# Kernel optimization log

Hardware: AMD Instinct MI355X
Metric: run time of the kernel (lower is better)

## Reference

```python
import jax, jax.numpy as jnp
import numpy as np

N, E = 100_000, 1_600_000
C_IN = C_OUT = 2


def _ln(h, g, b, eps=1e-5):
    mu = h.mean(-1, keepdims=True)
    var = ((h - mu) ** 2).mean(-1, keepdims=True)
    return (h - mu) * jax.lax.rsqrt(var + eps) * g + b


def _radial(x, W1, b1, g1, be1, W2, b2, g2, be2, W3, b3):
    h = jax.nn.relu(_ln(x @ W1 + b1, g1, be1))
    h = jax.nn.relu(_ln(h @ W2 + b2, g2, be2))
    return h @ W3 + b3


def setup_inputs() -> dict:
    key = jax.random.key(0)
    ks = jax.random.split(key, 20)
    inp = {
        "f0": jax.random.normal(ks[0], (N, C_IN, 1), jnp.float32),
        "f1": jax.random.normal(ks[1], (N, C_IN, 3), jnp.float32),
        "dist": jax.random.uniform(ks[2], (E,), jnp.float32),
        "u": jax.random.randint(ks[3], (E,), 0, N),
        "v": jax.random.randint(ks[4], (E,), 0, N),
        "wq": 0.5 * jax.random.normal(ks[5], (2, C_OUT, C_IN), jnp.float32),
        "wj00": jax.random.normal(ks[6], (E, 1, 1, 1), jnp.float32),
        "wj01": jax.random.normal(ks[7], (E, 1, 1, 3), jnp.float32),
        "wj10": jax.random.normal(ks[8], (E, 1, 3, 1), jnp.float32),
        "wj11": jax.random.normal(ks[9], (E, 3, 3, 3), jnp.float32),
        # radial MLP params for the 4 WLayers, index i = 2*l + k
        "rW1": 0.5 * jax.random.normal(ks[10], (4, C_IN + 1, 16), jnp.float32),
        "rb1": jnp.zeros((4, 16), jnp.float32),
        "g1": jnp.ones((4, 16), jnp.float32),
        "be1": jnp.zeros((4, 16), jnp.float32),
        "rW2": 0.3 * jax.random.normal(ks[11], (4, 16, 16), jnp.float32),
        "rb2": jnp.zeros((4, 16), jnp.float32),
        "g2": jnp.ones((4, 16), jnp.float32),
        "be2": jnp.zeros((4, 16), jnp.float32),
        "W3_00": 0.3 * jax.random.normal(ks[12], (16, 4), jnp.float32),
        "b3_00": jnp.zeros((4,), jnp.float32),
        "W3_01": 0.3 * jax.random.normal(ks[13], (16, 4), jnp.float32),
        "b3_01": jnp.zeros((4,), jnp.float32),
        "W3_10": 0.3 * jax.random.normal(ks[14], (16, 4), jnp.float32),
        "b3_10": jnp.zeros((4,), jnp.float32),
        "W3_11": 0.3 * jax.random.normal(ks[15], (16, 12), jnp.float32),
        "b3_11": jnp.zeros((12,), jnp.float32),
    }
    return inp


def reference(f0, f1, dist, u, v, wq, wj00, wj01, wj10, wj11,
              rW1, rb1, g1, be1, rW2, rb2, g2, be2,
              W3_00, b3_00, W3_01, b3_01, W3_10, b3_10, W3_11, b3_11):
    n = f0.shape[0]
    e = u.shape[0]
    # calc_q: [N, c_out, sum(2k+1)=4]
    q = jnp.concatenate([jnp.einsum('oi,nik->nok', wq[0], f0),
                         jnp.einsum('oi,nik->nok', wq[1], f1)], axis=2)
    # per-edge radial input: [dot(f0_src, f0_dst) over rep dim, dist] -> [E, c_in+1]
    vec = jnp.concatenate([jnp.sum(f0[u] * f0[v], axis=2), dist[:, None]], axis=1)
    f_dst = (f0[v], f1[v])  # edges.dst[k]
    wjs = {(0, 0): wj00, (0, 1): wj01, (1, 0): wj10, (1, 1): wj11}
    W3s = {(0, 0): (W3_00, b3_00), (0, 1): (W3_01, b3_01),
           (1, 0): (W3_10, b3_10), (1, 1): (W3_11, b3_11)}
    # calc_k: for each output degree l, sum over input degrees k of
    #   einsum('ejoi,ejlk,eik->eol', R, w_j, f_dst[k])  (fused form of the
    #   original 'ejoi,ejlk->eoilk' then 'eoilk,eik->eol')
    kl = []
    for l in range(2):
        acc = jnp.zeros((e, C_OUT, 2 * l + 1), f0.dtype)
        for k in range(2):
            i = 2 * l + k
            W3, b3 = W3s[(l, k)]
            J = 2 * min(k, l) + 1
            R = _radial(vec, rW1[i], rb1[i], g1[i], be1[i],
                        rW2[i], rb2[i], g2[i], be2[i], W3, b3)
            R = R.reshape(e, J, C_OUT, C_IN)
            acc = acc + jnp.einsum('ejoi,ejlk,eik->eol', R, wjs[(l, k)], f_dst[k])
        kl.append(acc)
    k_feat = jnp.concatenate(kl, axis=2)  # [E, c_out, 4]
    dot = jnp.einsum('eol,eol->e', q[v], k_feat)  # [E]
    # scatter logsumexp over destination nodes, then edge softmax weights
    m = jax.lax.stop_gradient(jax.ops.segment_max(dot, v, num_segments=n))
    m = jnp.where(jnp.isfinite(m), m, 0.0)
    ssum = jax.ops.segment_sum(jnp.exp(dot - m[v]), v, num_segments=n)
    lse = m + jnp.log(ssum)
    return jnp.exp(dot - lse[v])
```

## Files before the change

### kernel.cpp

```cpp
#include <hip/hip_runtime.h>
#include <math.h>


#define TPB 256
#define EPB 128

typedef float f2 __attribute__((ext_vector_type(2)));
typedef float f4 __attribute__((ext_vector_type(4)));

static __device__ __forceinline__ f2 fma2(f2 a, f2 b, f2 c) {
    return __builtin_elementwise_fma(a, b, c);
}
static __device__ __forceinline__ f2 splat(float x) {
    f2 r;
    r.x = x;
    r.y = x;
    return r;
}
static __device__ __forceinline__ f2 mk2(float a, float b) {
    f2 r;
    r.x = a;
    r.y = b;
    return r;
}

static __device__ __forceinline__ void ln_relu_pair(f2* h,
                                                    const float* __restrict__ g,
                                                    const float* __restrict__ be) {
    f2 s = ((h[0] + h[1]) + (h[2] + h[3])) + ((h[4] + h[5]) + (h[6] + h[7])) +
           (((h[8] + h[9]) + (h[10] + h[11])) +
            ((h[12] + h[13]) + (h[14] + h[15])));
    const f2 mu = s * splat(0.0625f);
    f2 vs = splat(0.f);
#pragma unroll
    for (int c = 0; c < 16; ++c) {
        f2 d = h[c] - mu;
        vs = fma2(d, d, vs);
    }
    const f2 var = vs * splat(0.0625f);
    f2 r;
    r.x = rsqrtf(var.x + 1e-5f);
    r.y = rsqrtf(var.y + 1e-5f);
    const f2 zero = splat(0.f);
#pragma unroll
    for (int c = 0; c < 16; ++c) {
        f2 t = (h[c] - mu) * r;
        h[c] = __builtin_elementwise_max(fma2(t, splat(g[c]), splat(be[c])), zero);
    }
}

static __device__ __forceinline__ void radial_pair(
    f2 v0, f2 v1, f2 v2, const float* __restrict__ W1,
    const float* __restrict__ b1, const float* __restrict__ g1,
    const float* __restrict__ be1, const float* __restrict__ W2,
    const float* __restrict__ b2, const float* __restrict__ g2,
    const float* __restrict__ be2, f2* h2) {
    f2 h[16];
#pragma unroll
    for (int c = 0; c < 16; ++c)
        h[c] = fma2(v0, splat(W1[c]),
                    fma2(v1, splat(W1[16 + c]),
                         fma2(v2, splat(W1[32 + c]), splat(b1[c]))));
    ln_relu_pair(h, g1, be1);

#pragma unroll
    for (int c2 = 0; c2 < 16; ++c2) h2[c2] = splat(b2[c2]);
#pragma unroll
    for (int c = 0; c < 16; ++c) {
#pragma unroll
        for (int c2 = 0; c2 < 16; ++c2)
            h2[c2] = fma2(h[c], splat(W2[c * 16 + c2]), h2[c2]);
    }
    ln_relu_pair(h2, g2, be2);
}

static __device__ __forceinline__ void layer3_pair4(const f2* h2,
                                                    const float* __restrict__ W3,
                                                    const float* __restrict__ b3,
                                                    f2 p[4]) {
#pragma unroll
    for (int oi = 0; oi < 4; ++oi) p[oi] = splat(b3[oi]);
#pragma unroll
    for (int c = 0; c < 16; ++c) {
#pragma unroll
        for (int oi = 0; oi < 4; ++oi)
            p[oi] = fma2(h2[c], splat(W3[c * 4 + oi]), p[oi]);
    }
}

__global__ __launch_bounds__(TPB, 4) void edge_kernel(
    const float* __restrict__ f0, const float* __restrict__ f1,
    const float* __restrict__ dist, const int* __restrict__ u,
    const int* __restrict__ v, const float* __restrict__ wq,
    const float* __restrict__ wj00, const float* __restrict__ wj01,
    const float* __restrict__ wj10, const float* __restrict__ wj11,
    const float* __restrict__ rW1, const float* __restrict__ rb1,
    const float* __restrict__ g1, const float* __restrict__ be1,
    const float* __restrict__ rW2, const float* __restrict__ rb2,
    const float* __restrict__ g2, const float* __restrict__ be2,
    const float* __restrict__ W3_00, const float* __restrict__ b3_00,
    const float* __restrict__ W3_01, const float* __restrict__ b3_01,
    const float* __restrict__ W3_10, const float* __restrict__ b3_10,
    const float* __restrict__ W3_11, const float* __restrict__ b3_11,
    float* __restrict__ out, double* __restrict__ ssum, int E) {
    __shared__ __align__(16) float s11[EPB * 27];
    __shared__ __align__(16) float s01[EPB * 3];
    __shared__ __align__(16) float s10[EPB * 3];
    __shared__ __align__(16) float sprep[EPB * 12];
    __shared__ int sv[EPB];
    __shared__ f2 pdot[4][64];

    const int tid = threadIdx.x;
    const int base = blockIdx.x * EPB;
    const int rem = E - base;
    const int nE = (rem < EPB) ? rem : EPB;

    if (nE == EPB) {
        const f4* s11s = (const f4*)(wj11 + (size_t)base * 27);
        f4* s11d = (f4*)s11;
#pragma unroll 2
        for (int i = tid; i < EPB * 27 / 4; i += TPB) s11d[i] = s11s[i];
        if (tid < EPB * 3 / 4) {
            ((f4*)s01)[tid] = ((const f4*)(wj01 + (size_t)base * 3))[tid];
            ((f4*)s10)[tid] = ((const f4*)(wj10 + (size_t)base * 3))[tid];
        }
    } else {
        for (int i = tid; i < EPB * 27; i += TPB)
            s11[i] = (i < nE * 27) ? wj11[(size_t)base * 27 + i] : 0.f;
        for (int i = tid; i < EPB * 3; i += TPB) {
            s01[i] = (i < nE * 3) ? wj01[(size_t)base * 3 + i] : 0.f;
            s10[i] = (i < nE * 3) ? wj10[(size_t)base * 3 + i] : 0.f;
        }
    }

    if (tid < EPB) {
        const int e = base + tid;
        f4 t0 = {0.f, 0.f, 0.f, 0.f};
        f4 t1 = {0.f, 0.f, 0.f, 0.f};
        f4 t2 = {0.f, 0.f, 0.f, 0.f};
        int vv = 0;
        if (e < E) {
            const int uu = u[e];
            vv = v[e];
            const f2 f0u = *(const f2*)(f0 + (size_t)uu * 2);
            const f2 f0v2 = *(const f2*)(f0 + (size_t)vv * 2);
            const f2 f1a = *(const f2*)(f1 + (size_t)vv * 6);
            const f2 f1b = *(const f2*)(f1 + (size_t)vv * 6 + 2);
            const f2 f1c = *(const f2*)(f1 + (size_t)vv * 6 + 4);
            const float d = dist[e];
            t0.x = f0u.x * f0v2.x;
            t0.y = f0u.y * f0v2.y;
            t0.z = d;
            t0.w = f0v2.x;
            t1.x = f0v2.y;
            t1.y = f1a.x;
            t1.z = f1a.y;
            t1.w = f1b.x;
            t2.x = f1b.y;
            t2.y = f1c.x;
            t2.z = f1c.y;
        }
        f4* dst = (f4*)(sprep + tid * 12);
        dst[0] = t0;
        dst[1] = t1;
        dst[2] = t2;
        sv[tid] = vv;
    }
    __syncthreads();

    const int l = tid & 63;
    const int w = __builtin_amdgcn_readfirstlane(tid >> 6);

    const float* pA = sprep + l * 12;
    const float* pB = sprep + (l + 64) * 12;
#define PR(k) mk2(pA[k], pB[k])
    const f2 vec0 = PR(0);
    const f2 vec1 = PR(1);
    const f2 vec2 = PR(2);
    const f2 f0v0 = PR(3);
    const f2 f0v1 = PR(4);
    f2 f1v[2][3];
    if (w != 0) {
        f1v[0][0] = PR(5);
        f1v[0][1] = PR(6);
        f1v[0][2] = PR(7);
        f1v[1][0] = PR(8);
        f1v[1][1] = PR(9);
        f1v[1][2] = PR(10);
    }
#undef PR

    f2 h2[16];
    radial_pair(vec0, vec1, vec2, rW1 + w * 48, rb1 + w * 16, g1 + w * 16,
                be1 + w * 16, rW2 + w * 256, rb2 + w * 16, g2 + w * 16,
                be2 + w * 16, h2);

    f2 dotp = splat(0.f);
    if (w == 0) {
        f2 p[4];
        layer3_pair4(h2, W3_00, b3_00, p);
        const int eA = base + l, eB = eA + 64;
        f2 wj;
        wj.x = (eA < E) ? wj00[eA] : 0.f;
        wj.y = (eB < E) ? wj00[eB] : 0.f;
        const f2 a0 = wj * fma2(p[0], f0v0, p[1] * f0v1);
        const f2 a1 = wj * fma2(p[2], f0v0, p[3] * f0v1);
        const f2 q00 = fma2(splat(wq[0]), f0v0, splat(wq[1]) * f0v1);
        const f2 q01 = fma2(splat(wq[2]), f0v0, splat(wq[3]) * f0v1);
        dotp = fma2(q00, a0, q01 * a1);
    } else if (w == 1) {
        f2 p[4];
        layer3_pair4(h2, W3_01, b3_01, p);
        const float* mA = s01 + l * 3;
        const float* mB = s01 + (l + 64) * 3;
        f2 s0 = splat(0.f), s1 = splat(0.f);
#pragma unroll
        for (int m = 0; m < 3; ++m) {
            const f2 wm = mk2(mA[m], mB[m]);
            s0 = fma2(wm, f1v[0][m], s0);
            s1 = fma2(wm, f1v[1][m], s1);
        }
        const f2 a0 = fma2(p[0], s0, p[1] * s1);
        const f2 a1 = fma2(p[2], s0, p[3] * s1);
        const f2 q00 = fma2(splat(wq[0]), f0v0, splat(wq[1]) * f0v1);
        const f2 q01 = fma2(splat(wq[2]), f0v0, splat(wq[3]) * f0v1);
        dotp = fma2(q00, a0, q01 * a1);
    } else if (w == 2) {
        f2 p[4];
        layer3_pair4(h2, W3_10, b3_10, p);
        const f2 t0 = fma2(p[0], f0v0, p[1] * f0v1);
        const f2 t1 = fma2(p[2], f0v0, p[3] * f0v1);
        const float* mA = s10 + l * 3;
        const float* mB = s10 + (l + 64) * 3;
#pragma unroll
        for (int m = 0; m < 3; ++m) {
            const f2 wm = mk2(mA[m], mB[m]);
            const f2 q0 = fma2(splat(wq[4]), f1v[0][m], splat(wq[5]) * f1v[1][m]);
            const f2 q1 = fma2(splat(wq[6]), f1v[0][m], splat(wq[7]) * f1v[1][m]);
            dotp = fma2(q0 * wm, t0, dotp);
            dotp = fma2(q1 * wm, t1, dotp);
        }
    } else {
        f2 p[3][4];
#pragma unroll
        for (int j = 0; j < 3; ++j)
#pragma unroll
            for (int oi = 0; oi < 4; ++oi) p[j][oi] = splat(b3_11[j * 4 + oi]);
#pragma unroll
        for (int c = 0; c < 16; ++c) {
#pragma unroll
            for (int j = 0; j < 3; ++j)
#pragma unroll
                for (int oi = 0; oi < 4; ++oi)
                    p[j][oi] = fma2(h2[c], splat(W3_11[c * 12 + j * 4 + oi]),
                                    p[j][oi]);
        }
        const float* mA = s11 + l * 27;
        const float* mB = s11 + (l + 64) * 27;
        f2 acc1[2][3];
#pragma unroll
        for (int m = 0; m < 3; ++m) {
            acc1[0][m] = splat(0.f);
            acc1[1][m] = splat(0.f);
        }
#pragma unroll
        for (int j = 0; j < 3; ++j) {
#pragma unroll
            for (int m = 0; m < 3; ++m) {
                const f2 w0 = mk2(mA[j * 9 + m * 3 + 0], mB[j * 9 + m * 3 + 0]);
                const f2 w1 = mk2(mA[j * 9 + m * 3 + 1], mB[j * 9 + m * 3 + 1]);
                const f2 w2 = mk2(mA[j * 9 + m * 3 + 2], mB[j * 9 + m * 3 + 2]);
                const f2 B0 =
                    fma2(w0, f1v[0][0], fma2(w1, f1v[0][1], w2 * f1v[0][2]));
                const f2 B1 =
                    fma2(w0, f1v[1][0], fma2(w1, f1v[1][1], w2 * f1v[1][2]));
                acc1[0][m] = fma2(p[j][0], B0, fma2(p[j][1], B1, acc1[0][m]));
                acc1[1][m] = fma2(p[j][2], B0, fma2(p[j][3], B1, acc1[1][m]));
            }
        }
#pragma unroll
        for (int m = 0; m < 3; ++m) {
            const f2 q0 = fma2(splat(wq[4]), f1v[0][m], splat(wq[5]) * f1v[1][m]);
            const f2 q1 = fma2(splat(wq[6]), f1v[0][m], splat(wq[7]) * f1v[1][m]);
            dotp = fma2(q0, acc1[0][m], dotp);
            dotp = fma2(q1, acc1[1][m], dotp);
        }
    }

    pdot[w][l] = dotp;
    __syncthreads();

    if (w == 0) {
        const f2 d =
            (pdot[0][l] + pdot[1][l]) + (pdot[2][l] + pdot[3][l]);
        const int eA = base + l, eB = eA + 64;
        if (eA < E) {
            out[eA] = d.x;
            atomicAdd(&ssum[sv[l]], exp((double)d.x));
        }
        if (eB < E) {
            out[eB] = d.y;
            atomicAdd(&ssum[sv[l + 64]], exp((double)d.y));
        }
    }
}

__global__ void norm_kernel(float* __restrict__ out, const int* __restrict__ v,
                            const double* __restrict__ ssum, int E) {
    int e = blockIdx.x * blockDim.x + threadIdx.x;
    if (e >= E) return;
    const double t = exp((double)out[e]);
    out[e] = (float)(t / ssum[v[e]]);
}

extern "C" void kernel_launch(void* const* d_in, const int* in_sizes, int n_in,
                              void* d_out, int out_size, void* d_ws,
                              size_t ws_size, hipStream_t stream) {
    const float* f0 = (const float*)d_in[0];
    const float* f1 = (const float*)d_in[1];
    const float* dist = (const float*)d_in[2];
    const int* u = (const int*)d_in[3];
    const int* v = (const int*)d_in[4];
    const float* wq = (const float*)d_in[5];
    const float* wj00 = (const float*)d_in[6];
    const float* wj01 = (const float*)d_in[7];
    const float* wj10 = (const float*)d_in[8];
    const float* wj11 = (const float*)d_in[9];
    const float* rW1 = (const float*)d_in[10];
    const float* rb1 = (const float*)d_in[11];
    const float* g1 = (const float*)d_in[12];
    const float* be1 = (const float*)d_in[13];
    const float* rW2 = (const float*)d_in[14];
    const float* rb2 = (const float*)d_in[15];
    const float* g2 = (const float*)d_in[16];
    const float* be2 = (const float*)d_in[17];
    const float* W3_00 = (const float*)d_in[18];
    const float* b3_00 = (const float*)d_in[19];
    const float* W3_01 = (const float*)d_in[20];
    const float* b3_01 = (const float*)d_in[21];
    const float* W3_10 = (const float*)d_in[22];
    const float* b3_10 = (const float*)d_in[23];
    const float* W3_11 = (const float*)d_in[24];
    const float* b3_11 = (const float*)d_in[25];

    const int N = in_sizes[0] / 2;
    const int E = in_sizes[2];

    double* ssum = (double*)d_ws;
    float* out = (float*)d_out;

    hipMemsetAsync(ssum, 0, (size_t)N * sizeof(double), stream);
    const int ge = (E + EPB - 1) / EPB;
    edge_kernel<<<ge, TPB, 0, stream>>>(
        f0, f1, dist, u, v, wq, wj00, wj01, wj10, wj11, rW1, rb1, g1, be1, rW2,
        rb2, g2, be2, W3_00, b3_00, W3_01, b3_01, W3_10, b3_10, W3_11, b3_11,
        out, ssum, E);
    const int gn = (E + TPB - 1) / TPB;
    norm_kernel<<<gn, TPB, 0, stream>>>(out, v, ssum, E);
}
```

Measured before the change: 406.1 us.

## Halve block to two waves, each computing two radial MLPs interleaved

The edge block drops from four wavefronts (one radial MLP each) to two. Each wave evaluates two radial MLPs side by side: wave 0 pairs (0,0) with (1,1), wave 1 pairs (0,1) with (1,0), which balances the heavier 11 path. The interleaved dual MLP is meant to give more independent FMAs per thread for ILP. The prep shared buffer becomes structure-of-arrays so all 128 threads write it without bank conflicts. The trade is higher register pressure and a lower occupancy hint (3 instead of 4), with less wave-level parallelism per edge tile.

```diff
diff --git a/kernel.cpp b/kernel.cpp
--- a/kernel.cpp
+++ b/kernel.cpp
@@ -2,7 +2,7 @@
 #include <math.h>
 
 
-#define TPB 256
+#define TPB 128
 #define EPB 128
 
 typedef float f2 __attribute__((ext_vector_type(2)));
@@ -24,54 +24,77 @@
     return r;
 }
 
-static __device__ __forceinline__ void ln_relu_pair(f2* h,
-                                                    const float* __restrict__ g,
-                                                    const float* __restrict__ be) {
-    f2 s = ((h[0] + h[1]) + (h[2] + h[3])) + ((h[4] + h[5]) + (h[6] + h[7])) +
-           (((h[8] + h[9]) + (h[10] + h[11])) +
-            ((h[12] + h[13]) + (h[14] + h[15])));
-    const f2 mu = s * splat(0.0625f);
-    f2 vs = splat(0.f);
-#pragma unroll
-    for (int c = 0; c < 16; ++c) {
-        f2 d = h[c] - mu;
-        vs = fma2(d, d, vs);
-    }
-    const f2 var = vs * splat(0.0625f);
-    f2 r;
-    r.x = rsqrtf(var.x + 1e-5f);
-    r.y = rsqrtf(var.y + 1e-5f);
+static __device__ __forceinline__ void ln_relu_dual(
+    f2* a, const float* __restrict__ ga, const float* __restrict__ ba,
+    f2* b, const float* __restrict__ gb, const float* __restrict__ bb) {
+    f2 sa = ((a[0] + a[1]) + (a[2] + a[3])) + ((a[4] + a[5]) + (a[6] + a[7])) +
+            (((a[8] + a[9]) + (a[10] + a[11])) +
+             ((a[12] + a[13]) + (a[14] + a[15])));
+    f2 sb = ((b[0] + b[1]) + (b[2] + b[3])) + ((b[4] + b[5]) + (b[6] + b[7])) +
+            (((b[8] + b[9]) + (b[10] + b[11])) +
+             ((b[12] + b[13]) + (b[14] + b[15])));
+    const f2 mua = sa * splat(0.0625f);
+    const f2 mub = sb * splat(0.0625f);
+    f2 va = splat(0.f), vb = splat(0.f);
+#pragma unroll
+    for (int c = 0; c < 16; ++c) {
+        f2 da = a[c] - mua;
+        f2 db = b[c] - mub;
+        va = fma2(da, da, va);
+        vb = fma2(db, db, vb);
+    }
+    const f2 vara = va * splat(0.0625f);
+    const f2 varb = vb * splat(0.0625f);
+    f2 ra, rb;
+    ra.x = rsqrtf(vara.x + 1e-5f);
+    ra.y = rsqrtf(vara.y + 1e-5f);
+    rb.x = rsqrtf(varb.x + 1e-5f);
+    rb.y = rsqrtf(varb.y + 1e-5f);
     const f2 zero = splat(0.f);
 #pragma unroll
     for (int c = 0; c < 16; ++c) {
-        f2 t = (h[c] - mu) * r;
-        h[c] = __builtin_elementwise_max(fma2(t, splat(g[c]), splat(be[c])), zero);
-    }
-}
-
-static __device__ __forceinline__ void radial_pair(
-    f2 v0, f2 v1, f2 v2, const float* __restrict__ W1,
-    const float* __restrict__ b1, const float* __restrict__ g1,
-    const float* __restrict__ be1, const float* __restrict__ W2,
-    const float* __restrict__ b2, const float* __restrict__ g2,
-    const float* __restrict__ be2, f2* h2) {
-    f2 h[16];
-#pragma unroll
-    for (int c = 0; c < 16; ++c)
-        h[c] = fma2(v0, splat(W1[c]),
-                    fma2(v1, splat(W1[16 + c]),
-                         fma2(v2, splat(W1[32 + c]), splat(b1[c]))));
-    ln_relu_pair(h, g1, be1);
-
-#pragma unroll
-    for (int c2 = 0; c2 < 16; ++c2) h2[c2] = splat(b2[c2]);
-#pragma unroll
-    for (int c = 0; c < 16; ++c) {
-#pragma unroll
-        for (int c2 = 0; c2 < 16; ++c2)
-            h2[c2] = fma2(h[c], splat(W2[c * 16 + c2]), h2[c2]);
-    }
-    ln_relu_pair(h2, g2, be2);
+        f2 ta = (a[c] - mua) * ra;
+        f2 tb = (b[c] - mub) * rb;
+        a[c] = __builtin_elementwise_max(fma2(ta, splat(ga[c]), splat(ba[c])), zero);
+        b[c] = __builtin_elementwise_max(fma2(tb, splat(gb[c]), splat(bb[c])), zero);
+    }
+}
+
+static __device__ __forceinline__ void radial_dual(
+    f2 v0, f2 v1, f2 v2, const float* __restrict__ W1A,
+    const float* __restrict__ b1A, const float* __restrict__ g1A,
+    const float* __restrict__ be1A, const float* __restrict__ W2A,
+    const float* __restrict__ b2A, const float* __restrict__ g2A,
+    const float* __restrict__ be2A, const float* __restrict__ W1B,
+    const float* __restrict__ b1B, const float* __restrict__ g1B,
+    const float* __restrict__ be1B, const float* __restrict__ W2B,
+    const float* __restrict__ b2B, const float* __restrict__ g2B,
+    const float* __restrict__ be2B, f2* h2a, f2* h2b) {
+    f2 ha[16], hb[16];
+#pragma unroll
+    for (int c = 0; c < 16; ++c) {
+        ha[c] = fma2(v0, splat(W1A[c]),
+                     fma2(v1, splat(W1A[16 + c]),
+                          fma2(v2, splat(W1A[32 + c]), splat(b1A[c]))));
+        hb[c] = fma2(v0, splat(W1B[c]),
+                     fma2(v1, splat(W1B[16 + c]),
+                          fma2(v2, splat(W1B[32 + c]), splat(b1B[c]))));
+    }
+    ln_relu_dual(ha, g1A, be1A, hb, g1B, be1B);
+#pragma unroll
+    for (int c2 = 0; c2 < 16; ++c2) {
+        h2a[c2] = splat(b2A[c2]);
+        h2b[c2] = splat(b2B[c2]);
+    }
+#pragma unroll
+    for (int c = 0; c < 16; ++c) {
+#pragma unroll
+        for (int c2 = 0; c2 < 16; ++c2) {
+            h2a[c2] = fma2(ha[c], splat(W2A[c * 16 + c2]), h2a[c2]);
+            h2b[c2] = fma2(hb[c], splat(W2B[c * 16 + c2]), h2b[c2]);
+        }
+    }
+    ln_relu_dual(h2a, g2A, be2A, h2b, g2B, be2B);
 }
 
 static __device__ __forceinline__ void layer3_pair4(const f2* h2,
@@ -88,7 +111,7 @@
     }
 }
 
-__global__ __launch_bounds__(TPB, 4) void edge_kernel(
+__global__ __launch_bounds__(TPB, 3) void edge_kernel(
     const float* __restrict__ f0, const float* __restrict__ f1,
     const float* __restrict__ dist, const int* __restrict__ u,
     const int* __restrict__ v, const float* __restrict__ wq,
@@ -106,9 +129,9 @@
     __shared__ __align__(16) float s11[EPB * 27];
     __shared__ __align__(16) float s01[EPB * 3];
     __shared__ __align__(16) float s10[EPB * 3];
-    __shared__ __align__(16) float sprep[EPB * 12];
+    __shared__ float sprep[11][EPB];
     __shared__ int sv[EPB];
-    __shared__ f2 pdot[4][64];
+    __shared__ f2 pdot[2][64];
 
     const int tid = threadIdx.x;
     const int base = blockIdx.x * EPB;
@@ -118,7 +141,6 @@
     if (nE == EPB) {
         const f4* s11s = (const f4*)(wj11 + (size_t)base * 27);
         f4* s11d = (f4*)s11;
-#pragma unroll 2
         for (int i = tid; i < EPB * 27 / 4; i += TPB) s11d[i] = s11s[i];
         if (tid < EPB * 3 / 4) {
             ((f4*)s01)[tid] = ((const f4*)(wj01 + (size_t)base * 3))[tid];
@@ -133,11 +155,11 @@
         }
     }
 
-    if (tid < EPB) {
+    {
         const int e = base + tid;
-        f4 t0 = {0.f, 0.f, 0.f, 0.f};
-        f4 t1 = {0.f, 0.f, 0.f, 0.f};
-        f4 t2 = {0.f, 0.f, 0.f, 0.f};
+        float p[11];
+#pragma unroll
+        for (int k = 0; k < 11; ++k) p[k] = 0.f;
         int vv = 0;
         if (e < E) {
             const int uu = u[e];
@@ -147,23 +169,20 @@
             const f2 f1a = *(const f2*)(f1 + (size_t)vv * 6);
             const f2 f1b = *(const f2*)(f1 + (size_t)vv * 6 + 2);
             const f2 f1c = *(const f2*)(f1 + (size_t)vv * 6 + 4);
-            const float d = dist[e];
-            t0.x = f0u.x * f0v2.x;
-            t0.y = f0u.y * f0v2.y;
-            t0.z = d;
-            t0.w = f0v2.x;
-            t1.x = f0v2.y;
-            t1.y = f1a.x;
-            t1.z = f1a.y;
-            t1.w = f1b.x;
-            t2.x = f1b.y;
-            t2.y = f1c.x;
-            t2.z = f1c.y;
-        }
-        f4* dst = (f4*)(sprep + tid * 12);
-        dst[0] = t0;
-        dst[1] = t1;
-        dst[2] = t2;
+            p[0] = f0u.x * f0v2.x;
+            p[1] = f0u.y * f0v2.y;
+            p[2] = dist[e];
+            p[3] = f0v2.x;
+            p[4] = f0v2.y;
+            p[5] = f1a.x;
+            p[6] = f1a.y;
+            p[7] = f1b.x;
+            p[8] = f1b.y;
+            p[9] = f1c.x;
+            p[10] = f1c.y;
+        }
+#pragma unroll
+        for (int k = 0; k < 11; ++k) sprep[k][tid] = p[k];
         sv[tid] = vv;
     }
     __syncthreads();
@@ -171,119 +190,132 @@
     const int l = tid & 63;
     const int w = __builtin_amdgcn_readfirstlane(tid >> 6);
 
-    const float* pA = sprep + l * 12;
-    const float* pB = sprep + (l + 64) * 12;
-#define PR(k) mk2(pA[k], pB[k])
-    const f2 vec0 = PR(0);
-    const f2 vec1 = PR(1);
-    const f2 vec2 = PR(2);
-    const f2 f0v0 = PR(3);
-    const f2 f0v1 = PR(4);
+    const int iA = w;
+    const int iB = 3 - w;
+
+    const f2 vec0 = mk2(sprep[0][l], sprep[0][l + 64]);
+    const f2 vec1 = mk2(sprep[1][l], sprep[1][l + 64]);
+    const f2 vec2 = mk2(sprep[2][l], sprep[2][l + 64]);
+
+    f2 h2a[16], h2b[16];
+    radial_dual(vec0, vec1, vec2,
+                rW1 + iA * 48, rb1 + iA * 16, g1 + iA * 16, be1 + iA * 16,
+                rW2 + iA * 256, rb2 + iA * 16, g2 + iA * 16, be2 + iA * 16,
+                rW1 + iB * 48, rb1 + iB * 16, g1 + iB * 16, be1 + iB * 16,
+                rW2 + iB * 256, rb2 + iB * 16, g2 + iB * 16, be2 + iB * 16,
+                h2a, h2b);
+
+    const f2 f0v0 = mk2(sprep[3][l], sprep[3][l + 64]);
+    const f2 f0v1 = mk2(sprep[4][l], sprep[4][l + 64]);
     f2 f1v[2][3];
-    if (w != 0) {
-        f1v[0][0] = PR(5);
-        f1v[0][1] = PR(6);
-        f1v[0][2] = PR(7);
-        f1v[1][0] = PR(8);
-        f1v[1][1] = PR(9);
-        f1v[1][2] = PR(10);
-    }
-#undef PR
-
-    f2 h2[16];
-    radial_pair(vec0, vec1, vec2, rW1 + w * 48, rb1 + w * 16, g1 + w * 16,
-                be1 + w * 16, rW2 + w * 256, rb2 + w * 16, g2 + w * 16,
-                be2 + w * 16, h2);
-
+    f1v[0][0] = mk2(sprep[5][l], sprep[5][l + 64]);
+    f1v[0][1] = mk2(sprep[6][l], sprep[6][l + 64]);
+    f1v[0][2] = mk2(sprep[7][l], sprep[7][l + 64]);
+    f1v[1][0] = mk2(sprep[8][l], sprep[8][l + 64]);
+    f1v[1][1] = mk2(sprep[9][l], sprep[9][l + 64]);
+    f1v[1][2] = mk2(sprep[10][l], sprep[10][l + 64]);
+
+    const int eA = base + l, eB = eA + 64;
     f2 dotp = splat(0.f);
+
     if (w == 0) {
-        f2 p[4];
-        layer3_pair4(h2, W3_00, b3_00, p);
-        const int eA = base + l, eB = eA + 64;
-        f2 wj;
-        wj.x = (eA < E) ? wj00[eA] : 0.f;
-        wj.y = (eB < E) ? wj00[eB] : 0.f;
-        const f2 a0 = wj * fma2(p[0], f0v0, p[1] * f0v1);
-        const f2 a1 = wj * fma2(p[2], f0v0, p[3] * f0v1);
-        const f2 q00 = fma2(splat(wq[0]), f0v0, splat(wq[1]) * f0v1);
-        const f2 q01 = fma2(splat(wq[2]), f0v0, splat(wq[3]) * f0v1);
-        dotp = fma2(q00, a0, q01 * a1);
-    } else if (w == 1) {
-        f2 p[4];
-        layer3_pair4(h2, W3_01, b3_01, p);
-        const float* mA = s01 + l * 3;
-        const float* mB = s01 + (l + 64) * 3;
-        f2 s0 = splat(0.f), s1 = splat(0.f);
-#pragma unroll
-        for (int m = 0; m < 3; ++m) {
-            const f2 wm = mk2(mA[m], mB[m]);
-            s0 = fma2(wm, f1v[0][m], s0);
-            s1 = fma2(wm, f1v[1][m], s1);
-        }
-        const f2 a0 = fma2(p[0], s0, p[1] * s1);
-        const f2 a1 = fma2(p[2], s0, p[3] * s1);
-        const f2 q00 = fma2(splat(wq[0]), f0v0, splat(wq[1]) * f0v1);
-        const f2 q01 = fma2(splat(wq[2]), f0v0, splat(wq[3]) * f0v1);
-        dotp = fma2(q00, a0, q01 * a1);
-    } else if (w == 2) {
-        f2 p[4];
-        layer3_pair4(h2, W3_10, b3_10, p);
-        const f2 t0 = fma2(p[0], f0v0, p[1] * f0v1);
-        const f2 t1 = fma2(p[2], f0v0, p[3] * f0v1);
-        const float* mA = s10 + l * 3;
-        const float* mB = s10 + (l + 64) * 3;
-#pragma unroll
-        for (int m = 0; m < 3; ++m) {
-            const f2 wm = mk2(mA[m], mB[m]);
-            const f2 q0 = fma2(splat(wq[4]), f1v[0][m], splat(wq[5]) * f1v[1][m]);
-            const f2 q1 = fma2(splat(wq[6]), f1v[0][m], splat(wq[7]) * f1v[1][m]);
-            dotp = fma2(q0 * wm, t0, dotp);
-            dotp = fma2(q1 * wm, t1, dotp);
+        {
+            f2 p[4];
+            layer3_pair4(h2a, W3_00, b3_00, p);
+            f2 wj;
+            wj.x = (eA < E) ? wj00[eA] : 0.f;
+            wj.y = (eB < E) ? wj00[eB] : 0.f;
+            const f2 a0 = wj * fma2(p[0], f0v0, p[1] * f0v1);
+            const f2 a1 = wj * fma2(p[2], f0v0, p[3] * f0v1);
+            const f2 q00 = fma2(splat(wq[0]), f0v0, splat(wq[1]) * f0v1);
+            const f2 q01 = fma2(splat(wq[2]), f0v0, splat(wq[3]) * f0v1);
+            dotp = fma2(q00, a0, q01 * a1);
+        }
+        {
+            f2 p[3][4];
+#pragma unroll
+            for (int j = 0; j < 3; ++j)
+#pragma unroll
+                for (int oi = 0; oi < 4; ++oi)
+                    p[j][oi] = splat(b3_11[j * 4 + oi]);
+#pragma unroll
+            for (int c = 0; c < 16; ++c) {
+#pragma unroll
+                for (int j = 0; j < 3; ++j)
+#pragma unroll
+                    for (int oi = 0; oi < 4; ++oi)
+                        p[j][oi] = fma2(h2b[c], splat(W3_11[c * 12 + j * 4 + oi]),
+                                        p[j][oi]);
+            }
+            const float* mA = s11 + l * 27;
+            const float* mB = s11 + (l + 64) * 27;
+            f2 acc1[2][3];
+#pragma unroll
+            for (int m = 0; m < 3; ++m) {
+                acc1[0][m] = splat(0.f);
+                acc1[1][m] = splat(0.f);
+            }
+#pragma unroll
+            for (int j = 0; j < 3; ++j) {
+#pragma unroll
+                for (int m = 0; m < 3; ++m) {
+                    const f2 w0 = mk2(mA[j * 9 + m * 3 + 0], mB[j * 9 + m * 3 + 0]);
+                    const f2 w1 = mk2(mA[j * 9 + m * 3 + 1], mB[j * 9 + m * 3 + 1]);
+                    const f2 w2 = mk2(mA[j * 9 + m * 3 + 2], mB[j * 9 + m * 3 + 2]);
+                    const f2 B0 =
+                        fma2(w0, f1v[0][0], fma2(w1, f1v[0][1], w2 * f1v[0][2]));
+                    const f2 B1 =
+                        fma2(w0, f1v[1][0], fma2(w1, f1v[1][1], w2 * f1v[1][2]));
+                    acc1[0][m] = fma2(p[j][0], B0, fma2(p[j][1], B1, acc1[0][m]));
+                    acc1[1][m] = fma2(p[j][2], B0, fma2(p[j][3], B1, acc1[1][m]));
+                }
+            }
+#pragma unroll
+            for (int m = 0; m < 3; ++m) {
+                const f2 q0 =
+                    fma2(splat(wq[4]), f1v[0][m], splat(wq[5]) * f1v[1][m]);
+                const f2 q1 =
+                    fma2(splat(wq[6]), f1v[0][m], splat(wq[7]) * f1v[1][m]);
+                dotp = fma2(q0, acc1[0][m], dotp);
+                dotp = fma2(q1, acc1[1][m], dotp);
+            }
         }
     } else {
-        f2 p[3][4];
-#pragma unroll
-        for (int j = 0; j < 3; ++j)
-#pragma unroll
-            for (int oi = 0; oi < 4; ++oi) p[j][oi] = splat(b3_11[j * 4 + oi]);
-#pragma unroll
-        for (int c = 0; c < 16; ++c) {
-#pragma unroll
-            for (int j = 0; j < 3; ++j)
-#pragma unroll
-                for (int oi = 0; oi < 4; ++oi)
-                    p[j][oi] = fma2(h2[c], splat(W3_11[c * 12 + j * 4 + oi]),
-                                    p[j][oi]);
-        }
-        const float* mA = s11 + l * 27;
-        const float* mB = s11 + (l + 64) * 27;
-        f2 acc1[2][3];
-#pragma unroll
-        for (int m = 0; m < 3; ++m) {
-            acc1[0][m] = splat(0.f);
-            acc1[1][m] = splat(0.f);
-        }
-#pragma unroll
-        for (int j = 0; j < 3; ++j) {
+        {
+            f2 p[4];
+            layer3_pair4(h2a, W3_01, b3_01, p);
+            const float* mA = s01 + l * 3;
+            const float* mB = s01 + (l + 64) * 3;
+            f2 s0 = splat(0.f), s1 = splat(0.f);
 #pragma unroll
             for (int m = 0; m < 3; ++m) {
-                const f2 w0 = mk2(mA[j * 9 + m * 3 + 0], mB[j * 9 + m * 3 + 0]);
-                const f2 w1 = mk2(mA[j * 9 + m * 3 + 1], mB[j * 9 + m * 3 + 1]);
-                const f2 w2 = mk2(mA[j * 9 + m * 3 + 2], mB[j * 9 + m * 3 + 2]);
-                const f2 B0 =
-                    fma2(w0, f1v[0][0], fma2(w1, f1v[0][1], w2 * f1v[0][2]));
-                const f2 B1 =
-                    fma2(w0, f1v[1][0], fma2(w1, f1v[1][1], w2 * f1v[1][2]));
-                acc1[0][m] = fma2(p[j][0], B0, fma2(p[j][1], B1, acc1[0][m]));
-                acc1[1][m] = fma2(p[j][2], B0, fma2(p[j][3], B1, acc1[1][m]));
-            }
-        }
-#pragma unroll
-        for (int m = 0; m < 3; ++m) {
-            const f2 q0 = fma2(splat(wq[4]), f1v[0][m], splat(wq[5]) * f1v[1][m]);
-            const f2 q1 = fma2(splat(wq[6]), f1v[0][m], splat(wq[7]) * f1v[1][m]);
-            dotp = fma2(q0, acc1[0][m], dotp);
-            dotp = fma2(q1, acc1[1][m], dotp);
+                const f2 wm = mk2(mA[m], mB[m]);
+                s0 = fma2(wm, f1v[0][m], s0);
+                s1 = fma2(wm, f1v[1][m], s1);
+            }
+            const f2 a0 = fma2(p[0], s0, p[1] * s1);
+            const f2 a1 = fma2(p[2], s0, p[3] * s1);
+            const f2 q00 = fma2(splat(wq[0]), f0v0, splat(wq[1]) * f0v1);
+            const f2 q01 = fma2(splat(wq[2]), f0v0, splat(wq[3]) * f0v1);
+            dotp = fma2(q00, a0, q01 * a1);
+        }
+        {
+            f2 p[4];
+            layer3_pair4(h2b, W3_10, b3_10, p);
+            const f2 t0 = fma2(p[0], f0v0, p[1] * f0v1);
+            const f2 t1 = fma2(p[2], f0v0, p[3] * f0v1);
+            const float* mA = s10 + l * 3;
+            const float* mB = s10 + (l + 64) * 3;
+#pragma unroll
+            for (int m = 0; m < 3; ++m) {
+                const f2 wm = mk2(mA[m], mB[m]);
+                const f2 q0 =
+                    fma2(splat(wq[4]), f1v[0][m], splat(wq[5]) * f1v[1][m]);
+                const f2 q1 =
+                    fma2(splat(wq[6]), f1v[0][m], splat(wq[7]) * f1v[1][m]);
+                dotp = fma2(q0 * wm, t0, dotp);
+                dotp = fma2(q1 * wm, t1, dotp);
+            }
         }
     }
 
@@ -291,9 +323,7 @@
     __syncthreads();
 
     if (w == 0) {
-        const f2 d =
-            (pdot[0][l] + pdot[1][l]) + (pdot[2][l] + pdot[3][l]);
-        const int eA = base + l, eB = eA + 64;
+        const f2 d = pdot[0][l] + pdot[1][l];
         if (eA < E) {
             out[eA] = d.x;
             atomicAdd(&ssum[sv[l]], exp((double)d.x));
@@ -355,6 +385,6 @@
         f0, f1, dist, u, v, wq, wj00, wj01, wj10, wj11, rW1, rb1, g1, be1, rW2,
         rb2, g2, be2, W3_00, b3_00, W3_01, b3_01, W3_10, b3_10, W3_11, b3_11,
         out, ssum, E);
-    const int gn = (E + TPB - 1) / TPB;
-    norm_kernel<<<gn, TPB, 0, stream>>>(out, v, ssum, E);
-}
+    const int gn = (E + 255) / 256;
+    norm_kernel<<<gn, 256, 0, stream>>>(out, v, ssum, E);
+}
```

Result: slower. 438.6 us (+8.0%).

## Make edge kernel persistent with register-prefetched next-slab loads

Applied to the files above, without the earlier changes.

Turns the one-block-per-128-edges kernel into a persistent grid-stride loop capped at 1536 blocks. Each slab's wj tensors and gathered node features are prefetched into registers while the current slab computes, then written into one unified shared staging buffer. The goal is to hide global-load latency behind the radial-MLP math and avoid per-block launch overhead. The cost is extra register pressure from the prefetch struct, which may reduce occupancy under the 4-wave launch bound.

```diff
diff --git a/kernel.cpp b/kernel.cpp
--- a/kernel.cpp
+++ b/kernel.cpp
@@ -4,6 +4,10 @@
 
 #define TPB 256
 #define EPB 128
+#define S01F 3456
+#define S10F 3840
+#define S00F 4224
+#define NSLOT 1088
 
 typedef float f2 __attribute__((ext_vector_type(2)));
 typedef float f4 __attribute__((ext_vector_type(4)));
@@ -21,6 +25,20 @@
     f2 r;
     r.x = a;
     r.y = b;
+    return r;
+}
+
+static __device__ __forceinline__ f4 ldf4g(const float* __restrict__ p,
+                                           long fb, long lim) {
+    f4 r;
+    if (fb + 4 <= lim) {
+        r = *(const f4*)(p + fb);
+    } else {
+        r.x = (fb + 0 < lim) ? p[fb + 0] : 0.f;
+        r.y = (fb + 1 < lim) ? p[fb + 1] : 0.f;
+        r.z = (fb + 2 < lim) ? p[fb + 2] : 0.f;
+        r.w = (fb + 3 < lim) ? p[fb + 3] : 0.f;
+    }
     return r;
 }
 
@@ -85,6 +103,71 @@
 #pragma unroll
         for (int oi = 0; oi < 4; ++oi)
             p[oi] = fma2(h2[c], splat(W3[c * 4 + oi]), p[oi]);
+    }
+}
+
+struct SReg {
+    f4 a0, a1, a2, a3, ax;
+    float pp[11];
+    int vv;
+};
+
+static __device__ __forceinline__ void load_stage(
+    int S, int E, int tid, const float* __restrict__ f0,
+    const float* __restrict__ f1, const float* __restrict__ dist,
+    const int* __restrict__ u, const int* __restrict__ v,
+    const float* __restrict__ wj00, const float* __restrict__ wj01,
+    const float* __restrict__ wj10, const float* __restrict__ wj11, SReg& r) {
+    const long sb = (long)S * EPB;
+    const long lim11 = (long)E * 27;
+    const long lim3 = (long)E * 3;
+    const long b11 = sb * 27;
+    const long b3 = sb * 3;
+    r.a0 = ldf4g(wj11, b11 + 4L * tid, lim11);
+    r.a1 = ldf4g(wj11, b11 + 4L * (tid + 256), lim11);
+    r.a2 = ldf4g(wj11, b11 + 4L * (tid + 512), lim11);
+    {
+        const int s3 = tid + 768;
+        if (s3 < 864)
+            r.a3 = ldf4g(wj11, b11 + 4L * s3, lim11);
+        else if (s3 < 960)
+            r.a3 = ldf4g(wj01, b3 + 4L * (s3 - 864), lim3);
+        else
+            r.a3 = ldf4g(wj10, b3 + 4L * (s3 - 960), lim3);
+    }
+    if (tid < 64) {
+        const int sx = 1024 + tid;
+        if (sx < 1056)
+            r.ax = ldf4g(wj10, b3 + 4L * (sx - 960), lim3);
+        else
+            r.ax = ldf4g(wj00, sb + 4L * (sx - 1056), (long)E);
+    }
+    if (tid >= 128) {
+        const int t = tid - 128;
+        const long e = sb + t;
+        r.vv = 0;
+#pragma unroll
+        for (int k = 0; k < 11; ++k) r.pp[k] = 0.f;
+        if (e < E) {
+            const int uu = u[e];
+            r.vv = v[e];
+            const f2 f0u = *(const f2*)(f0 + (size_t)uu * 2);
+            const f2 f0vv = *(const f2*)(f0 + (size_t)r.vv * 2);
+            const f2 f1a = *(const f2*)(f1 + (size_t)r.vv * 6);
+            const f2 f1b = *(const f2*)(f1 + (size_t)r.vv * 6 + 2);
+            const f2 f1c = *(const f2*)(f1 + (size_t)r.vv * 6 + 4);
+            r.pp[0] = f0u.x * f0vv.x;
+            r.pp[1] = f0u.y * f0vv.y;
+            r.pp[2] = dist[e];
+            r.pp[3] = f0vv.x;
+            r.pp[4] = f0vv.y;
+            r.pp[5] = f1a.x;
+            r.pp[6] = f1a.y;
+            r.pp[7] = f1b.x;
+            r.pp[8] = f1b.y;
+            r.pp[9] = f1c.x;
+            r.pp[10] = f1c.y;
+        }
     }
 }
 
@@ -103,205 +186,176 @@
     const float* __restrict__ W3_10, const float* __restrict__ b3_10,
     const float* __restrict__ W3_11, const float* __restrict__ b3_11,
     float* __restrict__ out, double* __restrict__ ssum, int E) {
-    __shared__ __align__(16) float s11[EPB * 27];
-    __shared__ __align__(16) float s01[EPB * 3];
-    __shared__ __align__(16) float s10[EPB * 3];
-    __shared__ __align__(16) float sprep[EPB * 12];
-    __shared__ int sv[EPB];
-    __shared__ f2 pdot[4][64];
+    __shared__ __align__(16) f4 sstage[NSLOT];
+    __shared__ float sprep[11][EPB];
+    __shared__ int sv[2][EPB];
+    __shared__ float pdotf[4][EPB];
 
     const int tid = threadIdx.x;
-    const int base = blockIdx.x * EPB;
-    const int rem = E - base;
-    const int nE = (rem < EPB) ? rem : EPB;
-
-    if (nE == EPB) {
-        const f4* s11s = (const f4*)(wj11 + (size_t)base * 27);
-        f4* s11d = (f4*)s11;
-#pragma unroll 2
-        for (int i = tid; i < EPB * 27 / 4; i += TPB) s11d[i] = s11s[i];
-        if (tid < EPB * 3 / 4) {
-            ((f4*)s01)[tid] = ((const f4*)(wj01 + (size_t)base * 3))[tid];
-            ((f4*)s10)[tid] = ((const f4*)(wj10 + (size_t)base * 3))[tid];
+    float* __restrict__ sf = (float*)sstage;
+    const int nslab = (E + EPB - 1) / EPB;
+
+    int s = blockIdx.x;
+    SReg r;
+    load_stage(s, E, tid, f0, f1, dist, u, v, wj00, wj01, wj10, wj11, r);
+    int par = 0;
+
+    while (s < nslab) {
+        sstage[tid] = r.a0;
+        sstage[tid + 256] = r.a1;
+        sstage[tid + 512] = r.a2;
+        sstage[tid + 768] = r.a3;
+        if (tid < 64) sstage[1024 + tid] = r.ax;
+        if (tid >= 128) {
+            const int t = tid - 128;
+#pragma unroll
+            for (int k = 0; k < 11; ++k) sprep[k][t] = r.pp[k];
+            sv[par][t] = r.vv;
         }
-    } else {
-        for (int i = tid; i < EPB * 27; i += TPB)
-            s11[i] = (i < nE * 27) ? wj11[(size_t)base * 27 + i] : 0.f;
-        for (int i = tid; i < EPB * 3; i += TPB) {
-            s01[i] = (i < nE * 3) ? wj01[(size_t)base * 3 + i] : 0.f;
-            s10[i] = (i < nE * 3) ? wj10[(size_t)base * 3 + i] : 0.f;
+        __syncthreads();
+
+        const int snext = s + (int)gridDim.x;
+        if (snext < nslab)
+            load_stage(snext, E, tid, f0, f1, dist, u, v, wj00, wj01, wj10,
+                       wj11, r);
+
+        const int l = tid & 63;
+        const int w = __builtin_amdgcn_readfirstlane(tid >> 6);
+
+        const f2 vec0 = mk2(sprep[0][l], sprep[0][l + 64]);
+        const f2 vec1 = mk2(sprep[1][l], sprep[1][l + 64]);
+        const f2 vec2 = mk2(sprep[2][l], sprep[2][l + 64]);
+
+        f2 h2[16];
+        radial_pair(vec0, vec1, vec2, rW1 + w * 48, rb1 + w * 16, g1 + w * 16,
+                    be1 + w * 16, rW2 + w * 256, rb2 + w * 16, g2 + w * 16,
+                    be2 + w * 16, h2);
+
+        const f2 f0v0 = mk2(sprep[3][l], sprep[3][l + 64]);
+        const f2 f0v1 = mk2(sprep[4][l], sprep[4][l + 64]);
+        f2 f1v[2][3];
+        if (w != 0) {
+            f1v[0][0] = mk2(sprep[5][l], sprep[5][l + 64]);
+            f1v[0][1] = mk2(sprep[6][l], sprep[6][l + 64]);
+            f1v[0][2] = mk2(sprep[7][l], sprep[7][l + 64]);
+            f1v[1][0] = mk2(sprep[8][l], sprep[8][l + 64]);
+            f1v[1][1] = mk2(sprep[9][l], sprep[9][l + 64]);
+            f1v[1][2] = mk2(sprep[10][l], sprep[10][l + 64]);
         }
-    }
-
-    if (tid < EPB) {
-        const int e = base + tid;
-        f4 t0 = {0.f, 0.f, 0.f, 0.f};
-        f4 t1 = {0.f, 0.f, 0.f, 0.f};
-        f4 t2 = {0.f, 0.f, 0.f, 0.f};
-        int vv = 0;
-        if (e < E) {
-            const int uu = u[e];
-            vv = v[e];
-            const f2 f0u = *(const f2*)(f0 + (size_t)uu * 2);
-            const f2 f0v2 = *(const f2*)(f0 + (size_t)vv * 2);
-            const f2 f1a = *(const f2*)(f1 + (size_t)vv * 6);
-            const f2 f1b = *(const f2*)(f1 + (size_t)vv * 6 + 2);
-            const f2 f1c = *(const f2*)(f1 + (size_t)vv * 6 + 4);
-            const float d = dist[e];
-            t0.x = f0u.x * f0v2.x;
-            t0.y = f0u.y * f0v2.y;
-            t0.z = d;
-            t0.w = f0v2.x;
-            t1.x = f0v2.y;
-            t1.y = f1a.x;
-            t1.z = f1a.y;
-            t1.w = f1b.x;
-            t2.x = f1b.y;
-            t2.y = f1c.x;
-            t2.z = f1c.y;
+
+        f2 dotp = splat(0.f);
+        if (w == 0) {
+            f2 p[4];
+            layer3_pair4(h2, W3_00, b3_00, p);
+            const f2 wj = mk2(sf[S00F + l], sf[S00F + l + 64]);
+            const f2 a0 = wj * fma2(p[0], f0v0, p[1] * f0v1);
+            const f2 a1 = wj * fma2(p[2], f0v0, p[3] * f0v1);
+            const f2 q00 = fma2(splat(wq[0]), f0v0, splat(wq[1]) * f0v1);
+            const f2 q01 = fma2(splat(wq[2]), f0v0, splat(wq[3]) * f0v1);
+            dotp = fma2(q00, a0, q01 * a1);
+        } else if (w == 1) {
+            f2 p[4];
+            layer3_pair4(h2, W3_01, b3_01, p);
+            const float* mA = sf + S01F + l * 3;
+            const float* mB = sf + S01F + (l + 64) * 3;
+            f2 s0 = splat(0.f), s1 = splat(0.f);
+#pragma unroll
+            for (int m = 0; m < 3; ++m) {
+                const f2 wm = mk2(mA[m], mB[m]);
+                s0 = fma2(wm, f1v[0][m], s0);
+                s1 = fma2(wm, f1v[1][m], s1);
+            }
+            const f2 a0 = fma2(p[0], s0, p[1] * s1);
+            const f2 a1 = fma2(p[2], s0, p[3] * s1);
+            const f2 q00 = fma2(splat(wq[0]), f0v0, splat(wq[1]) * f0v1);
+            const f2 q01 = fma2(splat(wq[2]), f0v0, splat(wq[3]) * f0v1);
+            dotp = fma2(q00, a0, q01 * a1);
+        } else if (w == 2) {
+            f2 p[4];
+            layer3_pair4(h2, W3_10, b3_10, p);
+            const f2 t0 = fma2(p[0], f0v0, p[1] * f0v1);
+            const f2 t1 = fma2(p[2], f0v0, p[3] * f0v1);
+            const float* mA = sf + S10F + l * 3;
+            const float* mB = sf + S10F + (l + 64) * 3;
+#pragma unroll
+            for (int m = 0; m < 3; ++m) {
+                const f2 wm = mk2(mA[m], mB[m]);
+                const f2 q0 =
+                    fma2(splat(wq[4]), f1v[0][m], splat(wq[5]) * f1v[1][m]);
+                const f2 q1 =
+                    fma2(splat(wq[6]), f1v[0][m], splat(wq[7]) * f1v[1][m]);
+                dotp = fma2(q0 * wm, t0, dotp);
+                dotp = fma2(q1 * wm, t1, dotp);
+            }
+        } else {
+            f2 p[3][4];
+#pragma unroll
+            for (int j = 0; j < 3; ++j)
+#pragma unroll
+                for (int oi = 0; oi < 4; ++oi)
+                    p[j][oi] = splat(b3_11[j * 4 + oi]);
+#pragma unroll
+            for (int c = 0; c < 16; ++c) {
+#pragma unroll
+                for (int j = 0; j < 3; ++j)
+#pragma unroll
+                    for (int oi = 0; oi < 4; ++oi)
+                        p[j][oi] = fma2(h2[c],
+                                        splat(W3_11[c * 12 + j * 4 + oi]),
+                                        p[j][oi]);
+            }
+            const float* mA = sf + l * 27;
+            const float* mB = sf + (l + 64) * 27;
+            f2 acc1[2][3];
+#pragma unroll
+            for (int m = 0; m < 3; ++m) {
+                acc1[0][m] = splat(0.f);
+                acc1[1][m] = splat(0.f);
+            }
+#pragma unroll
+            for (int j = 0; j < 3; ++j) {
+#pragma unroll
+                for (int m = 0; m < 3; ++m) {
+                    const f2 w0 =
+                        mk2(mA[j * 9 + m * 3 + 0], mB[j * 9 + m * 3 + 0]);
+                    const f2 w1 =
+                        mk2(mA[j * 9 + m * 3 + 1], mB[j * 9 + m * 3 + 1]);
+                    const f2 w2 =
+                        mk2(mA[j * 9 + m * 3 + 2], mB[j * 9 + m * 3 + 2]);
+                    const f2 B0 =
+                        fma2(w0, f1v[0][0], fma2(w1, f1v[0][1], w2 * f1v[0][2]));
+                    const f2 B1 =
+                        fma2(w0, f1v[1][0], fma2(w1, f1v[1][1], w2 * f1v[1][2]));
+                    acc1[0][m] = fma2(p[j][0], B0, fma2(p[j][1], B1, acc1[0][m]));
+                    acc1[1][m] = fma2(p[j][2], B0, fma2(p[j][3], B1, acc1[1][m]));
+                }
+            }
+#pragma unroll
+            for (int m = 0; m < 3; ++m) {
+                const f2 q0 =
+                    fma2(splat(wq[4]), f1v[0][m], splat(wq[5]) * f1v[1][m]);
+                const f2 q1 =
+                    fma2(splat(wq[6]), f1v[0][m], splat(wq[7]) * f1v[1][m]);
+                dotp = fma2(q0, acc1[0][m], dotp);
+                dotp = fma2(q1, acc1[1][m], dotp);
+            }
         }
-        f4* dst = (f4*)(sprep + tid * 12);
-        dst[0] = t0;
-        dst[1] = t1;
-        dst[2] = t2;
-        sv[tid] = vv;
-    }
-    __syncthreads();
-
-    const int l = tid & 63;
-    const int w = __builtin_amdgcn_readfirstlane(tid >> 6);
-
-    const float* pA = sprep + l * 12;
-    const float* pB = sprep + (l + 64) * 12;
-#define PR(k) mk2(pA[k], pB[k])
-    const f2 vec0 = PR(0);
-    const f2 vec1 = PR(1);
-    const f2 vec2 = PR(2);
-    const f2 f0v0 = PR(3);
-    const f2 f0v1 = PR(4);
-    f2 f1v[2][3];
-    if (w != 0) {
-        f1v[0][0] = PR(5);
-        f1v[0][1] = PR(6);
-        f1v[0][2] = PR(7);
-        f1v[1][0] = PR(8);
-        f1v[1][1] = PR(9);
-        f1v[1][2] = PR(10);
-    }
-#undef PR
-
-    f2 h2[16];
-    radial_pair(vec0, vec1, vec2, rW1 + w * 48, rb1 + w * 16, g1 + w * 16,
-                be1 + w * 16, rW2 + w * 256, rb2 + w * 16, g2 + w * 16,
-                be2 + w * 16, h2);
-
-    f2 dotp = splat(0.f);
-    if (w == 0) {
-        f2 p[4];
-        layer3_pair4(h2, W3_00, b3_00, p);
-        const int eA = base + l, eB = eA + 64;
-        f2 wj;
-        wj.x = (eA < E) ? wj00[eA] : 0.f;
-        wj.y = (eB < E) ? wj00[eB] : 0.f;
-        const f2 a0 = wj * fma2(p[0], f0v0, p[1] * f0v1);
-        const f2 a1 = wj * fma2(p[2], f0v0, p[3] * f0v1);
-        const f2 q00 = fma2(splat(wq[0]), f0v0, splat(wq[1]) * f0v1);
-        const f2 q01 = fma2(splat(wq[2]), f0v0, splat(wq[3]) * f0v1);
-        dotp = fma2(q00, a0, q01 * a1);
-    } else if (w == 1) {
-        f2 p[4];
-        layer3_pair4(h2, W3_01, b3_01, p);
-        const float* mA = s01 + l * 3;
-        const float* mB = s01 + (l + 64) * 3;
-        f2 s0 = splat(0.f), s1 = splat(0.f);
-#pragma unroll
-        for (int m = 0; m < 3; ++m) {
-            const f2 wm = mk2(mA[m], mB[m]);
-            s0 = fma2(wm, f1v[0][m], s0);
-            s1 = fma2(wm, f1v[1][m], s1);
+
+        pdotf[w][l] = dotp.x;
+        pdotf[w][l + 64] = dotp.y;
+        __syncthreads();
+
+        if (tid < EPB) {
+            const long e = (long)s * EPB + tid;
+            if (e < E) {
+                const float dsum = pdotf[0][tid] + pdotf[1][tid] +
+                                   pdotf[2][tid] + pdotf[3][tid];
+                out[e] = dsum;
+                atomicAdd(&ssum[sv[par][tid]], exp((double)dsum));
+            }
         }
-        const f2 a0 = fma2(p[0], s0, p[1] * s1);
-        const f2 a1 = fma2(p[2], s0, p[3] * s1);
-        const f2 q00 = fma2(splat(wq[0]), f0v0, splat(wq[1]) * f0v1);
-        const f2 q01 = fma2(splat(wq[2]), f0v0, splat(wq[3]) * f0v1);
-        dotp = fma2(q00, a0, q01 * a1);
-    } else if (w == 2) {
-        f2 p[4];
-        layer3_pair4(h2, W3_10, b3_10, p);
-        const f2 t0 = fma2(p[0], f0v0, p[1] * f0v1);
-        const f2 t1 = fma2(p[2], f0v0, p[3] * f0v1);
-        const float* mA = s10 + l * 3;
-        const float* mB = s10 + (l + 64) * 3;
-#pragma unroll
-        for (int m = 0; m < 3; ++m) {
-            const f2 wm = mk2(mA[m], mB[m]);
-            const f2 q0 = fma2(splat(wq[4]), f1v[0][m], splat(wq[5]) * f1v[1][m]);
-            const f2 q1 = fma2(splat(wq[6]), f1v[0][m], splat(wq[7]) * f1v[1][m]);
-            dotp = fma2(q0 * wm, t0, dotp);
-            dotp = fma2(q1 * wm, t1, dotp);
-        }
-    } else {
-        f2 p[3][4];
-#pragma unroll
-        for (int j = 0; j < 3; ++j)
-#pragma unroll
-            for (int oi = 0; oi < 4; ++oi) p[j][oi] = splat(b3_11[j * 4 + oi]);
-#pragma unroll
-        for (int c = 0; c < 16; ++c) {
-#pragma unroll
-            for (int j = 0; j < 3; ++j)
-#pragma unroll
-                for (int oi = 0; oi < 4; ++oi)
-                    p[j][oi] = fma2(h2[c], splat(W3_11[c * 12 + j * 4 + oi]),
-                                    p[j][oi]);
-        }
-        const float* mA = s11 + l * 27;
-        const float* mB = s11 + (l + 64) * 27;
-        f2 acc1[2][3];
-#pragma unroll
-        for (int m = 0; m < 3; ++m) {
-            acc1[0][m] = splat(0.f);
-            acc1[1][m] = splat(0.f);
-        }
-#pragma unroll
-        for (int j = 0; j < 3; ++j) {
-#pragma unroll
-            for (int m = 0; m < 3; ++m) {
-                const f2 w0 = mk2(mA[j * 9 + m * 3 + 0], mB[j * 9 + m * 3 + 0]);
-                const f2 w1 = mk2(mA[j * 9 + m * 3 + 1], mB[j * 9 + m * 3 + 1]);
-                const f2 w2 = mk2(mA[j * 9 + m * 3 + 2], mB[j * 9 + m * 3 + 2]);
-                const f2 B0 =
-                    fma2(w0, f1v[0][0], fma2(w1, f1v[0][1], w2 * f1v[0][2]));
-                const f2 B1 =
-                    fma2(w0, f1v[1][0], fma2(w1, f1v[1][1], w2 * f1v[1][2]));
-                acc1[0][m] = fma2(p[j][0], B0, fma2(p[j][1], B1, acc1[0][m]));
-                acc1[1][m] = fma2(p[j][2], B0, fma2(p[j][3], B1, acc1[1][m]));
-            }
-        }
-#pragma unroll
-        for (int m = 0; m < 3; ++m) {
-            const f2 q0 = fma2(splat(wq[4]), f1v[0][m], splat(wq[5]) * f1v[1][m]);
-            const f2 q1 = fma2(splat(wq[6]), f1v[0][m], splat(wq[7]) * f1v[1][m]);
-            dotp = fma2(q0, acc1[0][m], dotp);
-            dotp = fma2(q1, acc1[1][m], dotp);
-        }
-    }
-
-    pdot[w][l] = dotp;
-    __syncthreads();
-
-    if (w == 0) {
-        const f2 d =
-            (pdot[0][l] + pdot[1][l]) + (pdot[2][l] + pdot[3][l]);
-        const int eA = base + l, eB = eA + 64;
-        if (eA < E) {
-            out[eA] = d.x;
-            atomicAdd(&ssum[sv[l]], exp((double)d.x));
-        }
-        if (eB < E) {
-            out[eB] = d.y;
-            atomicAdd(&ssum[sv[l + 64]], exp((double)d.y));
-        }
+        s = snext;
+        par ^= 1;
     }
 }
 
@@ -350,11 +404,12 @@
     float* out = (float*)d_out;
 
     hipMemsetAsync(ssum, 0, (size_t)N * sizeof(double), stream);
-    const int ge = (E + EPB - 1) / EPB;
+    const int nslab = (E + EPB - 1) / EPB;
+    const int ge = nslab < 1536 ? nslab : 1536;
     edge_kernel<<<ge, TPB, 0, stream>>>(
         f0, f1, dist, u, v, wq, wj00, wj01, wj10, wj11, rW1, rb1, g1, be1, rW2,
         rb2, g2, be2, W3_00, b3_00, W3_01, b3_01, W3_10, b3_10, W3_11, b3_11,
         out, ssum, E);
-    const int gn = (E + TPB - 1) / TPB;
-    norm_kernel<<<gn, TPB, 0, stream>>>(out, v, ssum, E);
-}
+    const int gn = (E + 255) / 256;
+    norm_kernel<<<gn, 256, 0, stream>>>(out, v, ssum, E);
+}
```

Result: slower. 627.2 us (+54.4%).
